# Performance work log

Hardware: AMD Instinct MI355X
Metric: run time of the kernel (lower is better)

The kernel has to match this reference:

```python
import jax, jax.numpy as jnp
import numpy as np

HIDDEN = 4096
NUM_HEADS = 32
NUM_KV_HEADS = 8
HEAD_DIM = 128
ROTARY_DIM = HEAD_DIM // 2  # partial_rotary_factor = 0.5
ROPE_THETA = 10000.0
EPS = 1e-5
T = 2048
Q_SIZE = NUM_HEADS * HEAD_DIM      # 4096
KV_SIZE = NUM_KV_HEADS * HEAD_DIM  # 1024


def setup_inputs() -> dict:
    key = jax.random.key(0)
    ks = jax.random.split(key, 6)
    s_in = 1.0 / np.sqrt(HIDDEN)
    s_o = 1.0 / np.sqrt(Q_SIZE)
    return {
        "positions": jnp.arange(T, dtype=jnp.int64),
        "hidden_states": jax.random.normal(ks[0], (T, HIDDEN), dtype=jnp.float32),
        "w_qkv": jax.random.normal(ks[1], (Q_SIZE + 2 * KV_SIZE, HIDDEN), dtype=jnp.float32) * s_in,
        "b_qkv": jax.random.normal(ks[2], (Q_SIZE + 2 * KV_SIZE,), dtype=jnp.float32) * 0.02,
        "q_norm_w": jnp.ones((HEAD_DIM,), dtype=jnp.float32),
        "k_norm_w": jnp.ones((HEAD_DIM,), dtype=jnp.float32),
        "w_o": jax.random.normal(ks[3], (HIDDEN, Q_SIZE), dtype=jnp.float32) * s_o,
    }


def _rms_norm(x, w, eps=EPS):
    # x: [..., head_dim]
    var = jnp.mean(x * x, axis=-1, keepdims=True)
    return x * jax.lax.rsqrt(var + eps) * w


def _apply_rope(x, positions):
    # x: [T, H, head_dim]; NeoX-style rotation on first ROTARY_DIM dims
    half = ROTARY_DIM // 2
    inv_freq = 1.0 / (ROPE_THETA ** (jnp.arange(0, ROTARY_DIM, 2, dtype=jnp.float32) / ROTARY_DIM))
    freqs = positions.astype(jnp.float32)[:, None] * inv_freq[None, :]  # [T, half]
    cos = jnp.cos(freqs)[:, None, :]  # [T, 1, half]
    sin = jnp.sin(freqs)[:, None, :]
    x_rot, x_pass = x[..., :ROTARY_DIM], x[..., ROTARY_DIM:]
    x1, x2 = x_rot[..., :half], x_rot[..., half:]
    rot = jnp.concatenate([x1 * cos - x2 * sin, x2 * cos + x1 * sin], axis=-1)
    return jnp.concatenate([rot, x_pass], axis=-1)


def reference(positions, hidden_states, w_qkv, b_qkv, q_norm_w, k_norm_w, w_o):
    qkv = hidden_states @ w_qkv.T + b_qkv  # [T, Q+2KV]
    q = qkv[:, :Q_SIZE].reshape(T, NUM_HEADS, HEAD_DIM)
    k = qkv[:, Q_SIZE:Q_SIZE + KV_SIZE].reshape(T, NUM_KV_HEADS, HEAD_DIM)
    v = qkv[:, Q_SIZE + KV_SIZE:].reshape(T, NUM_KV_HEADS, HEAD_DIM)

    q = _rms_norm(q, q_norm_w)
    k = _rms_norm(k, k_norm_w)

    q = _apply_rope(q, positions)
    k = _apply_rope(k, positions)

    # GQA: expand kv heads to match q heads
    rep = NUM_HEADS // NUM_KV_HEADS
    k = jnp.repeat(k, rep, axis=1)  # [T, H, D]
    v = jnp.repeat(v, rep, axis=1)

    scale = HEAD_DIM ** -0.5
    scores = jnp.einsum('qhd,khd->hqk', q, k) * scale  # [H, T, T]
    causal = positions[:, None] >= positions[None, :]  # [T, T]
    scores = jnp.where(causal[None, :, :], scores, jnp.float32(-1e30))
    probs = jax.nn.softmax(scores, axis=-1)
    attn = jnp.einsum('hqk,khd->qhd', probs, v).reshape(T, Q_SIZE)
    return attn @ w_o.T
```

## Files before the change

### kernel.cpp

```cpp
#include <hip/hip_runtime.h>
#include <stdint.h>

#define T_SEQ 2048
#define HIDDEN 4096
#define NUM_HEADS 32
#define NUM_KV 8
#define HD 128
#define QSIZE (NUM_HEADS * HD)
#define KVSIZE (NUM_KV * HD)
#define QKV_N (QSIZE + 2 * KVSIZE)

typedef __attribute__((ext_vector_type(8))) __bf16 bf16x8;
typedef __attribute__((ext_vector_type(4))) float f32x4;

static __device__ __forceinline__ unsigned short f2bf(float f) {
  union { float f; unsigned int u; } v; v.f = f;
  unsigned int u = v.u;
  return (unsigned short)((u + 0x7FFFu + ((u >> 16) & 1u)) >> 16);
}

static __device__ __forceinline__ void async16(const void* g, void* l) {
  __builtin_amdgcn_global_load_lds((__attribute__((address_space(1))) void*)g,
                                   (__attribute__((address_space(3))) void*)l,
                                   16, 0, 0);
}

static __device__ __forceinline__ bf16x8 lds_frag(const unsigned short* p) {
  return *(const bf16x8*)p;
}

#define N1 (T_SEQ * HIDDEN / 4)
#define N2 (QKV_N * HIDDEN / 4)
#define N3 (HIDDEN * QSIZE / 4)
__global__ void cvt_all(const float* __restrict__ h,
                        const float* __restrict__ wq,
                        const float* __restrict__ wo,
                        unsigned short* __restrict__ hb,
                        unsigned short* __restrict__ wqb,
                        unsigned short* __restrict__ wob) {
  int i = blockIdx.x * 256 + threadIdx.x;
  const float* src;
  unsigned short* dst;
  int j;
  if (i < N1) { src = h; dst = hb; j = i; }
  else if (i < N1 + N2) { src = wq; dst = wqb; j = i - N1; }
  else { src = wo; dst = wob; j = i - N1 - N2; }
  float4 f = ((const float4*)src)[j];
  ushort4 o;
  o.x = f2bf(f.x); o.y = f2bf(f.y); o.z = f2bf(f.z); o.w = f2bf(f.w);
  ((ushort4*)dst)[j] = o;
}

__global__ __launch_bounds__(256) void gemm_bt(
    const unsigned short* __restrict__ A,
    const unsigned short* __restrict__ Bt,
    const float* __restrict__ bias,
    float* __restrict__ C, int M, int N, int K) {
  __shared__ unsigned short lds_a[128 * 32];
  __shared__ unsigned short lds_b[128 * 32];
  const int tid = threadIdx.x;
  const int wave = tid >> 6, lane = tid & 63;
  const int quad = lane >> 4, l16 = lane & 15;
  const int row0 = blockIdx.x * 128, col0 = blockIdx.y * 128;
  const int wm = (wave >> 1) * 64, wn = (wave & 1) * 64;

  f32x4 acc[4][4] = {};

  const int e0 = wave * 1024 + lane * 8;
  const int e1 = e0 + 512;
  const unsigned short* Ab0 = A + (size_t)(row0 + (e0 >> 5)) * K + (e0 & 31);
  const unsigned short* Ab1 = A + (size_t)(row0 + (e1 >> 5)) * K + (e1 & 31);
  const unsigned short* Bb0 = Bt + (size_t)(col0 + (e0 >> 5)) * K + (e0 & 31);
  const unsigned short* Bb1 = Bt + (size_t)(col0 + (e1 >> 5)) * K + (e1 & 31);
  unsigned short* la0 = lds_a + wave * 1024;
  unsigned short* la1 = la0 + 512;
  unsigned short* lb0 = lds_b + wave * 1024;
  unsigned short* lb1 = lb0 + 512;

  for (int k0 = 0; k0 < K; k0 += 32) {
    __syncthreads();
    async16(Ab0 + k0, la0);
    async16(Ab1 + k0, la1);
    async16(Bb0 + k0, lb0);
    async16(Bb1 + k0, lb1);
    __syncthreads();
    bf16x8 af[4], bfr[4];
#pragma unroll
    for (int mt = 0; mt < 4; mt++)
      af[mt] = lds_frag(lds_a + (wm + mt * 16 + l16) * 32 + quad * 8);
#pragma unroll
    for (int nt = 0; nt < 4; nt++)
      bfr[nt] = lds_frag(lds_b + (wn + nt * 16 + l16) * 32 + quad * 8);
#pragma unroll
    for (int mt = 0; mt < 4; mt++)
#pragma unroll
      for (int nt = 0; nt < 4; nt++)
        acc[mt][nt] = __builtin_amdgcn_mfma_f32_16x16x32_bf16(
            af[mt], bfr[nt], acc[mt][nt], 0, 0, 0);
  }

#pragma unroll
  for (int mt = 0; mt < 4; mt++) {
#pragma unroll
    for (int nt = 0; nt < 4; nt++) {
      const int c = col0 + wn + nt * 16 + l16;
      const float bv = bias ? bias[c] : 0.0f;
      const int rbase = row0 + wm + mt * 16 + quad * 4;
#pragma unroll
      for (int r = 0; r < 4; r++)
        C[(size_t)(rbase + r) * N + c] = acc[mt][nt][r] + bv;
    }
  }
}

__global__ __launch_bounds__(256) void gemm_bt_splitk(
    const unsigned short* __restrict__ A,
    const unsigned short* __restrict__ Bt,
    float* __restrict__ C0, float* __restrict__ C1,
    int M, int N, int K, int kslice) {
  __shared__ unsigned short lds_a[128 * 32];
  __shared__ unsigned short lds_b[128 * 32];
  const int tid = threadIdx.x;
  const int wave = tid >> 6, lane = tid & 63;
  const int quad = lane >> 4, l16 = lane & 15;
  const int row0 = blockIdx.x * 128, col0 = blockIdx.y * 128;
  const int kofs = blockIdx.z * kslice;
  float* __restrict__ C = blockIdx.z ? C1 : C0;
  const int wm = (wave >> 1) * 64, wn = (wave & 1) * 64;

  f32x4 acc[4][4] = {};

  const int e0 = wave * 1024 + lane * 8;
  const int e1 = e0 + 512;
  const unsigned short* Ab0 = A + (size_t)(row0 + (e0 >> 5)) * K + kofs + (e0 & 31);
  const unsigned short* Ab1 = A + (size_t)(row0 + (e1 >> 5)) * K + kofs + (e1 & 31);
  const unsigned short* Bb0 = Bt + (size_t)(col0 + (e0 >> 5)) * K + kofs + (e0 & 31);
  const unsigned short* Bb1 = Bt + (size_t)(col0 + (e1 >> 5)) * K + kofs + (e1 & 31);
  unsigned short* la0 = lds_a + wave * 1024;
  unsigned short* la1 = la0 + 512;
  unsigned short* lb0 = lds_b + wave * 1024;
  unsigned short* lb1 = lb0 + 512;

  for (int k0 = 0; k0 < kslice; k0 += 32) {
    __syncthreads();
    async16(Ab0 + k0, la0);
    async16(Ab1 + k0, la1);
    async16(Bb0 + k0, lb0);
    async16(Bb1 + k0, lb1);
    __syncthreads();
    bf16x8 af[4], bfr[4];
#pragma unroll
    for (int mt = 0; mt < 4; mt++)
      af[mt] = lds_frag(lds_a + (wm + mt * 16 + l16) * 32 + quad * 8);
#pragma unroll
    for (int nt = 0; nt < 4; nt++)
      bfr[nt] = lds_frag(lds_b + (wn + nt * 16 + l16) * 32 + quad * 8);
#pragma unroll
    for (int mt = 0; mt < 4; mt++)
#pragma unroll
      for (int nt = 0; nt < 4; nt++)
        acc[mt][nt] = __builtin_amdgcn_mfma_f32_16x16x32_bf16(
            af[mt], bfr[nt], acc[mt][nt], 0, 0, 0);
  }

#pragma unroll
  for (int mt = 0; mt < 4; mt++) {
#pragma unroll
    for (int nt = 0; nt < 4; nt++) {
      const int c = col0 + wn + nt * 16 + l16;
      const int rbase = row0 + wm + mt * 16 + quad * 4;
#pragma unroll
      for (int r = 0; r < 4; r++)
        C[(size_t)(rbase + r) * N + c] = acc[mt][nt][r];
    }
  }
}

__global__ void reduce_add(float* __restrict__ out,
                           const float* __restrict__ part, int n4) {
  int i = blockIdx.x * 256 + threadIdx.x;
  if (i >= n4) return;
  float4 a = ((const float4*)out)[i];
  float4 b = ((const float4*)part)[i];
  a.x += b.x; a.y += b.y; a.z += b.z; a.w += b.w;
  ((float4*)out)[i] = a;
}

__global__ __launch_bounds__(256) void norm_rope(
    const float* __restrict__ qkv,
    const float* __restrict__ qw,
    const float* __restrict__ kw,
    unsigned short* __restrict__ q,
    unsigned short* __restrict__ k) {
  const int t = blockIdx.x;
  const int wave = threadIdx.x >> 6, lane = threadIdx.x & 63;
#pragma unroll
  for (int it = 0; it < 10; it++) {
    const int slot = it * 4 + wave;
    const bool isq = slot < 32;
    const float* src = qkv + (size_t)t * QKV_N +
                       (isq ? slot * HD : QSIZE + (slot - 32) * HD);
    const float x0 = src[lane];
    const float x1 = src[lane + 64];
    float ss = x0 * x0 + x1 * x1;
#pragma unroll
    for (int m = 32; m >= 1; m >>= 1) ss += __shfl_xor(ss, m, 64);
    const float rn = rsqrtf(ss * (1.0f / 128.0f) + 1e-5f);
    const float* w = isq ? qw : kw;
    const float y0 = x0 * rn * w[lane];
    const float y1 = x1 * rn * w[lane + 64];
    const float p = __shfl_xor(y0, 32, 64);
    const int j = lane & 31;
    const float inv = exp2f(-(float)j * (13.28771237954945f / 32.0f));
    float s, c;
    sincosf((float)t * inv, &s, &c);
    const float r0 = (lane < 32) ? (y0 * c - p * s) : (y0 * c + p * s);
    unsigned short* dst = isq ? q + ((size_t)slot * T_SEQ + t) * HD
                              : k + ((size_t)(slot - 32) * T_SEQ + t) * HD;
    dst[lane] = f2bf(r0);
    dst[lane + 64] = f2bf(y1);
  }
}

__global__ __launch_bounds__(256) void transpose_v(
    const float* __restrict__ qkv, unsigned short* __restrict__ vt) {
  __shared__ unsigned short tile[64 * 136];
  const int kvh = blockIdx.x, tt = blockIdx.y;
  const int tid = threadIdx.x;
  {
    const int t_r = tid >> 2, d0 = (tid & 3) * 32;
    const float* src = qkv + (size_t)(tt * 64 + t_r) * QKV_N +
                       (QSIZE + KVSIZE) + kvh * HD + d0;
#pragma unroll
    for (int i = 0; i < 8; i++) {
      float4 f = ((const float4*)src)[i];
      unsigned short* dptr = tile + t_r * 136 + d0 + i * 4;
      dptr[0] = f2bf(f.x); dptr[1] = f2bf(f.y);
      dptr[2] = f2bf(f.z); dptr[3] = f2bf(f.w);
    }
  }
  __syncthreads();
  {
    const int d_r = tid >> 1, t0 = (tid & 1) * 32;
    unsigned short buf[32];
#pragma unroll
    for (int i = 0; i < 32; i++) buf[i] = tile[(t0 + i) * 136 + d_r];
    uint4* dst = (uint4*)(vt + ((size_t)kvh * HD + d_r) * T_SEQ + tt * 64 + t0);
#pragma unroll
    for (int i = 0; i < 4; i++) dst[i] = ((uint4*)buf)[i];
  }
}

#define BC 64
#define KCH 528
#define VCH 544
#define PST 72
__global__ __launch_bounds__(256) void attn_fwd(
    const unsigned short* __restrict__ Q,
    const unsigned short* __restrict__ K,
    const unsigned short* __restrict__ Vt,
    unsigned short* __restrict__ O) {
  __shared__ unsigned short lds_k[16 * KCH];
  __shared__ unsigned short lds_v[16 * VCH];
  __shared__ unsigned short lds_p[4 * 32 * PST];

  const int bx = blockIdx.x;
  const int qb = 15 - (bx >> 5);
  const int h = bx & 31;
  const int kvh = h >> 2;
  const int tid = threadIdx.x, wave = tid >> 6, lane = tid & 63;
  const int quad = lane >> 4, l16 = lane & 15;
  const int q0 = qb * 128;
  const int mrow0 = q0 + wave * 32;

  bf16x8 qf[2][4];
#pragma unroll
  for (int m = 0; m < 2; m++) {
    const unsigned short* qp =
        Q + ((size_t)h * T_SEQ + mrow0 + m * 16 + l16) * HD + quad * 8;
#pragma unroll
    for (int c2 = 0; c2 < 4; c2++) qf[m][c2] = *(const bf16x8*)(qp + c2 * 32);
  }

  f32x4 o_acc[2][8] = {};
  float lrow[2][4] = {};
  const float l2e_s = 1.4426950408889634f * 0.08838834764831845f;
  const float FMAX = 129.0f;
  const unsigned short* kb = K + (size_t)kvh * T_SEQ * HD;
  const unsigned short* vtb = Vt + (size_t)kvh * HD * T_SEQ;
  unsigned short* pbase = lds_p + wave * 32 * PST;

  const int nkt = 2 * (qb + 1);
  for (int kt = 0; kt < nkt; kt++) {
    const int kbase = kt * BC;
    __syncthreads();
#pragma unroll
    for (int cc = 0; cc < 4; cc++) {
      const int c = wave + cc * 4;
      async16(kb + (size_t)(kbase + c * 4 + (lane >> 4)) * HD + (lane & 15) * 8,
              lds_k + c * KCH + lane * 8);
      async16(vtb + (size_t)(c * 8 + (lane >> 3)) * T_SEQ + kbase + (lane & 7) * 8,
              lds_v + c * VCH + lane * 8);
    }
    __syncthreads();

    if (kbase > mrow0 + 31) continue;

    f32x4 s[2][4] = {};
#pragma unroll
    for (int c2 = 0; c2 < 4; c2++) {
#pragma unroll
      for (int nt = 0; nt < 4; nt++) {
        bf16x8 kf = lds_frag(lds_k + (nt * 4 + (l16 >> 2)) * KCH +
                             (l16 & 3) * 128 + c2 * 32 + quad * 8);
        s[0][nt] = __builtin_amdgcn_mfma_f32_16x16x32_bf16(qf[0][c2], kf, s[0][nt], 0, 0, 0);
        s[1][nt] = __builtin_amdgcn_mfma_f32_16x16x32_bf16(qf[1][c2], kf, s[1][nt], 0, 0, 0);
      }
    }

    const bool domask = (kbase + 63 > mrow0);
#pragma unroll
    for (int m = 0; m < 2; m++) {
#pragma unroll
      for (int r = 0; r < 4; r++) {
        const int row = mrow0 + m * 16 + quad * 4 + r;
        float ps = 0.f;
        unsigned short* pw = pbase + (m * 16 + quad * 4 + r) * PST + l16;
#pragma unroll
        for (int nt = 0; nt < 4; nt++) {
          float x = s[m][nt][r];
          if (domask && (kbase + nt * 16 + l16 > row)) x = -INFINITY;
          const float p = exp2f((x - FMAX) * l2e_s);
          ps += p;
          pw[nt * 16] = f2bf(p);
        }
        lrow[m][r] += ps;
      }
    }

#pragma unroll
    for (int ks = 0; ks < 2; ks++) {
      bf16x8 pa0 = lds_frag(pbase + l16 * PST + ks * 32 + quad * 8);
      bf16x8 pa1 = lds_frag(pbase + (16 + l16) * PST + ks * 32 + quad * 8);
#pragma unroll
      for (int dt = 0; dt < 8; dt++) {
        bf16x8 vf = lds_frag(lds_v + (dt * 2 + (l16 >> 3)) * VCH +
                             (l16 & 7) * 64 + ks * 32 + quad * 8);
        o_acc[0][dt] = __builtin_amdgcn_mfma_f32_16x16x32_bf16(pa0, vf, o_acc[0][dt], 0, 0, 0);
        o_acc[1][dt] = __builtin_amdgcn_mfma_f32_16x16x32_bf16(pa1, vf, o_acc[1][dt], 0, 0, 0);
      }
    }
  }

#pragma unroll
  for (int m = 0; m < 2; m++) {
#pragma unroll
    for (int r = 0; r < 4; r++) {
      float l = lrow[m][r];
#pragma unroll
      for (int msk = 1; msk < 16; msk <<= 1) l += __shfl_xor(l, msk, 16);
      const float inv = 1.0f / l;
      const int row = mrow0 + m * 16 + quad * 4 + r;
#pragma unroll
      for (int dt = 0; dt < 8; dt++)
        O[(size_t)row * QSIZE + h * HD + dt * 16 + l16] =
            f2bf(o_acc[m][dt][r] * inv);
    }
  }
}

extern "C" void kernel_launch(void* const* d_in, const int* in_sizes, int n_in,
                              void* d_out, int out_size, void* d_ws, size_t ws_size,
                              hipStream_t stream) {
  const float* hidden = (const float*)d_in[1];
  const float* w_qkv  = (const float*)d_in[2];
  const float* b_qkv  = (const float*)d_in[3];
  const float* q_norm = (const float*)d_in[4];
  const float* k_norm = (const float*)d_in[5];
  const float* w_o    = (const float*)d_in[6];
  float* out = (float*)d_out;

  char* ws = (char*)d_ws;
  unsigned short* hidden_bf = (unsigned short*)(ws + 0);
  unsigned short* wqkv_bf   = (unsigned short*)(ws + 16777216);
  unsigned short* wo_bf     = (unsigned short*)(ws + 67108864);
  float*          qkv_f32   = (float*)(ws + 100663296);
  unsigned short* q_bf      = (unsigned short*)(ws + 150994944);
  unsigned short* k_bf      = (unsigned short*)(ws + 167772160);
  unsigned short* vt_bf     = (unsigned short*)(ws + 171966464);
  unsigned short* attn_bf   = (unsigned short*)(ws + 176160768);
  float*          part_f32  = (float*)(ws + 100663296);

  cvt_all<<<(N1 + N2 + N3 + 255) / 256, 256, 0, stream>>>(
      hidden, w_qkv, w_o, hidden_bf, wqkv_bf, wo_bf);

  gemm_bt<<<dim3(T_SEQ / 128, QKV_N / 128), 256, 0, stream>>>(
      hidden_bf, wqkv_bf, b_qkv, qkv_f32, T_SEQ, QKV_N, HIDDEN);

  norm_rope<<<dim3(T_SEQ), 256, 0, stream>>>(
      qkv_f32, q_norm, k_norm, q_bf, k_bf);

  transpose_v<<<dim3(8, T_SEQ / 64), 256, 0, stream>>>(qkv_f32, vt_bf);

  attn_fwd<<<dim3(512), 256, 0, stream>>>(q_bf, k_bf, vt_bf, attn_bf);

  gemm_bt_splitk<<<dim3(T_SEQ / 128, HIDDEN / 128, 2), 256, 0, stream>>>(
      attn_bf, wo_bf, out, part_f32, T_SEQ, HIDDEN, QSIZE, QSIZE / 2);

  reduce_add<<<(T_SEQ * HIDDEN / 4 + 255) / 256, 256, 0, stream>>>(
      out, part_f32, T_SEQ * HIDDEN / 4);
}
```

Measured before the change: 610.2 us.

## Double-buffer attention K/V tiles with smaller key block and occupancy hints

Attention now prefetches the next K/V tile into a second LDS buffer while the current one is being used, and drops one barrier per iteration. The key block shrinks from 64 to 32 so the double buffer fits in LDS. The GEMM and attention kernels gain a min-blocks-per-CU launch bound to raise occupancy, which may force register spills. Halving the key block doubles the loop trip count and the per-iteration overhead. Correctness depends on the async loads having completed by the next barrier without an explicit wait for them.

```diff
diff --git a/kernel.cpp b/kernel.cpp
--- a/kernel.cpp
+++ b/kernel.cpp
@@ -51,7 +51,7 @@
   ((ushort4*)dst)[j] = o;
 }
 
-__global__ __launch_bounds__(256) void gemm_bt(
+__global__ __launch_bounds__(256, 3) void gemm_bt(
     const unsigned short* __restrict__ A,
     const unsigned short* __restrict__ Bt,
     const float* __restrict__ bias,
@@ -113,7 +113,7 @@
   }
 }
 
-__global__ __launch_bounds__(256) void gemm_bt_splitk(
+__global__ __launch_bounds__(256, 3) void gemm_bt_splitk(
     const unsigned short* __restrict__ A,
     const unsigned short* __restrict__ Bt,
     float* __restrict__ C0, float* __restrict__ C1,
@@ -251,17 +251,17 @@
   }
 }
 
-#define BC 64
+#define BC 32
 #define KCH 528
-#define VCH 544
-#define PST 72
-__global__ __launch_bounds__(256) void attn_fwd(
+#define VCH 528
+#define PST 40
+__global__ __launch_bounds__(256, 3) void attn_fwd(
     const unsigned short* __restrict__ Q,
     const unsigned short* __restrict__ K,
     const unsigned short* __restrict__ Vt,
     unsigned short* __restrict__ O) {
-  __shared__ unsigned short lds_k[16 * KCH];
-  __shared__ unsigned short lds_v[16 * VCH];
+  __shared__ unsigned short lds_k[2][8 * KCH];
+  __shared__ unsigned short lds_v[2][8 * VCH];
   __shared__ unsigned short lds_p[4 * 32 * PST];
 
   const int bx = blockIdx.x;
@@ -290,35 +290,49 @@
   const unsigned short* vtb = Vt + (size_t)kvh * HD * T_SEQ;
   unsigned short* pbase = lds_p + wave * 32 * PST;
 
-  const int nkt = 2 * (qb + 1);
+  const int krr = lane >> 4, krd = (lane & 15) * 8;
+  const int vrr = lane >> 2, vrk = (lane & 3) * 8;
+
+  const int nkt = 4 * (qb + 1);
+
+#pragma unroll
+  for (int cc = 0; cc < 2; cc++) {
+    const int c = wave + cc * 4;
+    async16(kb + (size_t)(c * 4 + krr) * HD + krd, lds_k[0] + c * KCH + lane * 8);
+    async16(vtb + (size_t)(c * 16 + vrr) * T_SEQ + vrk, lds_v[0] + c * VCH + lane * 8);
+  }
+
   for (int kt = 0; kt < nkt; kt++) {
+    const int cur = kt & 1;
     const int kbase = kt * BC;
     __syncthreads();
-#pragma unroll
-    for (int cc = 0; cc < 4; cc++) {
-      const int c = wave + cc * 4;
-      async16(kb + (size_t)(kbase + c * 4 + (lane >> 4)) * HD + (lane & 15) * 8,
-              lds_k + c * KCH + lane * 8);
-      async16(vtb + (size_t)(c * 8 + (lane >> 3)) * T_SEQ + kbase + (lane & 7) * 8,
-              lds_v + c * VCH + lane * 8);
-    }
-    __syncthreads();
+    if (kt + 1 < nkt) {
+      const int nb = kbase + BC;
+#pragma unroll
+      for (int cc = 0; cc < 2; cc++) {
+        const int c = wave + cc * 4;
+        async16(kb + (size_t)(nb + c * 4 + krr) * HD + krd,
+                lds_k[cur ^ 1] + c * KCH + lane * 8);
+        async16(vtb + (size_t)(c * 16 + vrr) * T_SEQ + nb + vrk,
+                lds_v[cur ^ 1] + c * VCH + lane * 8);
+      }
+    }
 
     if (kbase > mrow0 + 31) continue;
 
-    f32x4 s[2][4] = {};
+    f32x4 s[2][2] = {};
 #pragma unroll
     for (int c2 = 0; c2 < 4; c2++) {
 #pragma unroll
-      for (int nt = 0; nt < 4; nt++) {
-        bf16x8 kf = lds_frag(lds_k + (nt * 4 + (l16 >> 2)) * KCH +
+      for (int nt = 0; nt < 2; nt++) {
+        bf16x8 kf = lds_frag(lds_k[cur] + (nt * 4 + (l16 >> 2)) * KCH +
                              (l16 & 3) * 128 + c2 * 32 + quad * 8);
         s[0][nt] = __builtin_amdgcn_mfma_f32_16x16x32_bf16(qf[0][c2], kf, s[0][nt], 0, 0, 0);
         s[1][nt] = __builtin_amdgcn_mfma_f32_16x16x32_bf16(qf[1][c2], kf, s[1][nt], 0, 0, 0);
       }
     }
 
-    const bool domask = (kbase + 63 > mrow0);
+    const bool domask = (kbase + 31 > mrow0);
 #pragma unroll
     for (int m = 0; m < 2; m++) {
 #pragma unroll
@@ -327,7 +341,7 @@
         float ps = 0.f;
         unsigned short* pw = pbase + (m * 16 + quad * 4 + r) * PST + l16;
 #pragma unroll
-        for (int nt = 0; nt < 4; nt++) {
+        for (int nt = 0; nt < 2; nt++) {
           float x = s[m][nt][r];
           if (domask && (kbase + nt * 16 + l16 > row)) x = -INFINITY;
           const float p = exp2f((x - FMAX) * l2e_s);
@@ -338,17 +352,13 @@
       }
     }
 
-#pragma unroll
-    for (int ks = 0; ks < 2; ks++) {
-      bf16x8 pa0 = lds_frag(pbase + l16 * PST + ks * 32 + quad * 8);
-      bf16x8 pa1 = lds_frag(pbase + (16 + l16) * PST + ks * 32 + quad * 8);
-#pragma unroll
-      for (int dt = 0; dt < 8; dt++) {
-        bf16x8 vf = lds_frag(lds_v + (dt * 2 + (l16 >> 3)) * VCH +
-                             (l16 & 7) * 64 + ks * 32 + quad * 8);
-        o_acc[0][dt] = __builtin_amdgcn_mfma_f32_16x16x32_bf16(pa0, vf, o_acc[0][dt], 0, 0, 0);
-        o_acc[1][dt] = __builtin_amdgcn_mfma_f32_16x16x32_bf16(pa1, vf, o_acc[1][dt], 0, 0, 0);
-      }
+    bf16x8 pa0 = lds_frag(pbase + l16 * PST + quad * 8);
+    bf16x8 pa1 = lds_frag(pbase + (16 + l16) * PST + quad * 8);
+#pragma unroll
+    for (int dt = 0; dt < 8; dt++) {
+      bf16x8 vf = lds_frag(lds_v[cur] + dt * VCH + l16 * 32 + quad * 8);
+      o_acc[0][dt] = __builtin_amdgcn_mfma_f32_16x16x32_bf16(pa0, vf, o_acc[0][dt], 0, 0, 0);
+      o_acc[1][dt] = __builtin_amdgcn_mfma_f32_16x16x32_bf16(pa1, vf, o_acc[1][dt], 0, 0, 0);
     }
   }
 
```

Result: faster. 581.1 us (-4.8%).
